# Performance work log

Measured on AMD Instinct MI355X. Metric: run time of the kernel, lower is better.

Reference implementation:

```python
import jax, jax.numpy as jnp
import numpy as np

VOCAB = 200000
P = 1000
B = 64
L = 2048

def setup_inputs() -> dict:
    key = jax.random.key(0)
    k1, k2, k3, k4, k5 = jax.random.split(key, 5)
    tokens = jax.random.randint(k1, (B, L), 0, VOCAB, dtype=jnp.int64)
    lengths = jax.random.randint(k2, (B,), 1, L + 1, dtype=jnp.int64)
    emb_table = jax.random.normal(k3, (VOCAB, P), dtype=jnp.float32)
    W = jax.random.normal(k4, (1, P), dtype=jnp.float32) / np.sqrt(P)
    b = jax.random.normal(k5, (1,), dtype=jnp.float32)
    return {"tokens": tokens, "lengths": lengths, "emb_table": emb_table, "W": W, "b": b}

def reference(tokens, lengths, emb_table, W, b):
    # Nested -> padded-with-zeros -> mean over dim=1 divides by max_len L
    # (torch.mean on the padded tensor), NOT per-sequence length.
    mask = (jnp.arange(L)[None, :] < lengths[:, None]).astype(emb_table.dtype)  # [B, L]
    emb = emb_table[tokens]                      # [B, L, P] gather
    pooled = jnp.einsum('blp,bl->bp', emb, mask) / jnp.asarray(L, emb_table.dtype)  # [B, P]
    logits = jax.nn.sigmoid(pooled @ W.T + b)    # [B, 1]
    return logits.reshape(B)
```

## Files before the change

kernel.cpp:

```cpp
#include <hip/hip_runtime.h>


constexpr int B_ = 64;
constexpr int L_ = 2048;
constexpr int P_ = 1000;
constexpr int BPS = 32;
constexpr int BDIM = 256;
constexpr int WAVES = BDIM / 64;
constexpr int SLOTS_PER_BLOCK = L_ / BPS;
constexpr int SLOTS_PER_WAVE = SLOTS_PER_BLOCK / WAVES;

__global__ __launch_bounds__(BDIM) void pool_dot_kernel(
    const int* __restrict__ tokens,
    const int* __restrict__ lengths,
    const float* __restrict__ emb,
    const float* __restrict__ W,
    float* __restrict__ partial)
{
    const int blk   = blockIdx.x;
    const int seq   = blk / BPS;
    const int chunk = blk % BPS;
    const int lane  = threadIdx.x & 63;
    const int wave  = threadIdx.x >> 6;

    const int len = (int)lengths[seq];
    __shared__ float red[WAVES];

    float accl = 0.0f;
    const int wbase = chunk * SLOTS_PER_BLOCK + wave * SLOTS_PER_WAVE;
    if (wbase < len) {
        const float4* W4 = (const float4*)W;
        float4 wf[4];
        #pragma unroll
        for (int k = 0; k < 4; ++k) {
            const int j = lane + 64 * k;
            if (j < P_ / 4) wf[k] = W4[j];
            else            wf[k] = make_float4(0.f, 0.f, 0.f, 0.f);
        }
        const int tend = min(len, wbase + SLOTS_PER_WAVE);
        for (int t = wbase; t < tend; ++t) {
            const int row = tokens[seq * L_ + t];
            const float4* e4 = (const float4*)(emb + (size_t)row * P_);
            #pragma unroll
            for (int k = 0; k < 4; ++k) {
                const int j = lane + 64 * k;
                if (j < P_ / 4) {
                    const float4 e = e4[j];
                    accl = fmaf(e.x, wf[k].x, accl);
                    accl = fmaf(e.y, wf[k].y, accl);
                    accl = fmaf(e.z, wf[k].z, accl);
                    accl = fmaf(e.w, wf[k].w, accl);
                }
            }
        }
    }

    #pragma unroll
    for (int off = 32; off > 0; off >>= 1)
        accl += __shfl_down(accl, off, 64);
    if (lane == 0) red[wave] = accl;
    __syncthreads();
    if (threadIdx.x == 0) {
        float s = 0.0f;
        #pragma unroll
        for (int w = 0; w < WAVES; ++w) s += red[w];
        partial[blk] = s;
    }
}

__global__ void finalize_kernel(const float* __restrict__ partial,
                                const float* __restrict__ bias,
                                float* __restrict__ out)
{
    const int i = threadIdx.x;
    if (i < B_) {
        float s = 0.0f;
        #pragma unroll
        for (int c = 0; c < BPS; ++c) s += partial[i * BPS + c];
        const float v = s * (1.0f / (float)L_) + bias[0];
        out[i] = 1.0f / (1.0f + expf(-v));
    }
}

extern "C" void kernel_launch(void* const* d_in, const int* in_sizes, int n_in,
                              void* d_out, int out_size, void* d_ws, size_t ws_size,
                              hipStream_t stream) {
    const int*   tokens  = (const int*)d_in[0];
    const int*   lengths = (const int*)d_in[1];
    const float* emb     = (const float*)d_in[2];
    const float* W       = (const float*)d_in[3];
    const float* bias    = (const float*)d_in[4];
    float* out     = (float*)d_out;
    float* partial = (float*)d_ws;

    pool_dot_kernel<<<B_ * BPS, BDIM, 0, stream>>>(tokens, lengths, emb, W, partial);
    finalize_kernel<<<1, 64, 0, stream>>>(partial, bias, out);
}
```

Measured before the change: 53.90 us.

## Interleave token slots across blocks and waves to balance variable-length work

Each sequence is now split across 64 blocks, and tokens are assigned round-robin with stride 256 (block chunk plus 64 per wave) instead of contiguous ranges. The goal is even work across blocks and waves regardless of sequence length, so blocks past the length no longer sit idle while others handle full chunks. The finalize step becomes one wave per sequence reducing its 64 partials with shuffles. The cost is twice as many blocks and scattered token index reads.

```diff
diff --git a/kernel.cpp b/kernel.cpp
--- a/kernel.cpp
+++ b/kernel.cpp
@@ -4,11 +4,9 @@
 constexpr int B_ = 64;
 constexpr int L_ = 2048;
 constexpr int P_ = 1000;
-constexpr int BPS = 32;
+constexpr int CPS = 64;
 constexpr int BDIM = 256;
 constexpr int WAVES = BDIM / 64;
-constexpr int SLOTS_PER_BLOCK = L_ / BPS;
-constexpr int SLOTS_PER_WAVE = SLOTS_PER_BLOCK / WAVES;
 
 __global__ __launch_bounds__(BDIM) void pool_dot_kernel(
     const int* __restrict__ tokens,
@@ -18,8 +16,8 @@
     float* __restrict__ partial)
 {
     const int blk   = blockIdx.x;
-    const int seq   = blk / BPS;
-    const int chunk = blk % BPS;
+    const int seq   = blk >> 6;
+    const int chunk = blk & (CPS - 1);
     const int lane  = threadIdx.x & 63;
     const int wave  = threadIdx.x >> 6;
 
@@ -27,8 +25,10 @@
     __shared__ float red[WAVES];
 
     float accl = 0.0f;
-    const int wbase = chunk * SLOTS_PER_BLOCK + wave * SLOTS_PER_WAVE;
-    if (wbase < len) {
+    const int t0 = chunk + 64 * wave;
+    const int nm = (t0 < len) ? (((len - 1 - t0) >> 8) + 1) : 0;
+
+    if (nm > 0) {
         const float4* W4 = (const float4*)W;
         float4 wf[4];
         #pragma unroll
@@ -37,9 +37,10 @@
             if (j < P_ / 4) wf[k] = W4[j];
             else            wf[k] = make_float4(0.f, 0.f, 0.f, 0.f);
         }
-        const int tend = min(len, wbase + SLOTS_PER_WAVE);
-        for (int t = wbase; t < tend; ++t) {
-            const int row = tokens[seq * L_ + t];
+        const int* trow = tokens + seq * L_;
+        for (int m = 0; m < nm; ++m) {
+            const int t   = t0 + (m << 8);
+            const int row = trow[t];
             const float4* e4 = (const float4*)(emb + (size_t)row * P_);
             #pragma unroll
             for (int k = 0; k < 4; ++k) {
@@ -72,13 +73,15 @@
                                 const float* __restrict__ bias,
                                 float* __restrict__ out)
 {
-    const int i = threadIdx.x;
-    if (i < B_) {
-        float s = 0.0f;
-        #pragma unroll
-        for (int c = 0; c < BPS; ++c) s += partial[i * BPS + c];
+    const int seq  = blockIdx.x;
+    const int lane = threadIdx.x;
+    float s = partial[seq * CPS + lane];
+    #pragma unroll
+    for (int off = 32; off > 0; off >>= 1)
+        s += __shfl_down(s, off, 64);
+    if (lane == 0) {
         const float v = s * (1.0f / (float)L_) + bias[0];
-        out[i] = 1.0f / (1.0f + expf(-v));
+        out[seq] = 1.0f / (1.0f + expf(-v));
     }
 }
 
@@ -93,6 +96,6 @@
     float* out     = (float*)d_out;
     float* partial = (float*)d_ws;
 
-    pool_dot_kernel<<<B_ * BPS, BDIM, 0, stream>>>(tokens, lengths, emb, W, partial);
-    finalize_kernel<<<1, 64, 0, stream>>>(partial, bias, out);
+    pool_dot_kernel<<<B_ * CPS, BDIM, 0, stream>>>(tokens, lengths, emb, W, partial);
+    finalize_kernel<<<B_, 64, 0, stream>>>(partial, bias, out);
 }
```

After: 48.36 us. 1.11x faster.
